# Performance work log

Hardware: AMD Instinct MI355X
Metric: run time of the kernel (lower is better)

Reference implementation:

```python
import jax, jax.numpy as jnp
import numpy as np

P, K, N, D = 4, 3, 250000, 64  # n_paths, num_powers, n_nodes, dim
N_EDGES = 100000


def setup_inputs() -> dict:
    key = jax.random.key(0)
    k1, k2, k3, k4 = jax.random.split(key, 4)
    feats = jax.random.normal(k1, (P, K, N, D), dtype=jnp.float32)
    # Each (path, power) slice was L2-normalized per node row in the original.
    feats = feats / jnp.linalg.norm(feats, axis=-1, keepdims=True)
    feature_weights = jnp.ones((P, K), dtype=jnp.float32)  # nn.Parameter init = ones
    intercept = jnp.float32(0.0)
    idx_i = jax.random.randint(k2, (N_EDGES,), 0, N, dtype=jnp.int64)
    idx_j = jax.random.randint(k3, (N_EDGES,), 0, N, dtype=jnp.int64)
    return {
        "precomputed_features": feats,
        "feature_weights": feature_weights,
        "intercept": intercept,
        "idx_i": idx_i,
        "idx_j": idx_j,
    }


def reference(precomputed_features, feature_weights, intercept, idx_i, idx_j):
    # softmax over the num_powers axis (dim=1 in torch)
    w = jax.nn.softmax(feature_weights, axis=1)  # [P, K]
    # weighted sum over paths and powers -> [N, D] embedding table
    emb = jnp.einsum("pk,pknd->nd", w, precomputed_features)
    zi = emb[idx_i]  # [E, D]
    zj = emb[idx_j]  # [E, D]
    dim = precomputed_features.shape[-1]
    dist_sq = jnp.sum((zi - zj) ** 2, axis=-1)
    logits = intercept - dist_sq / dim
    return jax.nn.sigmoid(logits)
```

## Files before the change

kernel.cpp:

```cpp
#include <hip/hip_runtime.h>
#include <hip/hip_bf16.h>
#include <math.h>


constexpr int Pp = 4;
constexpr int Kk = 3;
constexpr int Nn = 250000;
constexpr int Dd = 64;

__global__ __launch_bounds__(256) void fastrp_edge_kernel(
    const float* __restrict__ feats,
    const float* __restrict__ fw,
    const float* __restrict__ intercept,
    const int*   __restrict__ idx_i,
    const int*   __restrict__ idx_j,
    float*       __restrict__ out,
    int E)
{
    const int wave = (int)((blockIdx.x * (size_t)blockDim.x + threadIdx.x) >> 6);
    const int lane = threadIdx.x & 63;
    if (wave >= E) return;

    float w[Pp * Kk];
    #pragma unroll
    for (int p = 0; p < Pp; ++p) {
        float e[Kk];
        float m = -INFINITY;
        #pragma unroll
        for (int k = 0; k < Kk; ++k) {
            e[k] = fw[p * Kk + k];
            m = fmaxf(m, e[k]);
        }
        float s = 0.0f;
        #pragma unroll
        for (int k = 0; k < Kk; ++k) {
            e[k] = __expf(e[k] - m);
            s += e[k];
        }
        const float inv = 1.0f / s;
        #pragma unroll
        for (int k = 0; k < Kk; ++k) w[p * Kk + k] = e[k] * inv;
    }

    const long long i = (long long)idx_i[wave];
    const long long j = (long long)idx_j[wave];

    float zi = 0.0f, zj = 0.0f;
    #pragma unroll
    for (int pk = 0; pk < Pp * Kk; ++pk) {
        const float* base = feats + (size_t)pk * Nn * Dd;
        const float ai = base[i * Dd + lane];
        const float aj = base[j * Dd + lane];
        zi = fmaf(w[pk], ai, zi);
        zj = fmaf(w[pk], aj, zj);
    }

    float diff = zi - zj;
    float v = diff * diff;

    #pragma unroll
    for (int off = 32; off > 0; off >>= 1) {
        v += __shfl_xor(v, off, 64);
    }

    if (lane == 0) {
        const float logit = intercept[0] - v * (1.0f / Dd);
        out[wave] = 1.0f / (1.0f + __expf(-logit));
    }
}

extern "C" void kernel_launch(void* const* d_in, const int* in_sizes, int n_in,
                              void* d_out, int out_size, void* d_ws, size_t ws_size,
                              hipStream_t stream) {
    const float* feats     = (const float*)d_in[0];
    const float* fw        = (const float*)d_in[1];
    const float* intercept = (const float*)d_in[2];
    const int*   idx_i     = (const int*)d_in[3];
    const int*   idx_j     = (const int*)d_in[4];
    float*       out       = (float*)d_out;

    const int E = in_sizes[3];

    const int block = 256;
    const int waves_per_block = block / 64;
    const int grid = (E + waves_per_block - 1) / waves_per_block;

    fastrp_edge_kernel<<<grid, block, 0, stream>>>(feats, fw, intercept,
                                                   idx_i, idx_j, out, E);
}
```

Measured before the change: 909.6 us.

## Materialize weighted embedding table then gather edges with float4 loads

Splits the work into two kernels. The first streams all path/power feature slices once with float4 loads and writes a single softmax-weighted [N, D] embedding table into the workspace. The second gathers only that table per edge, with 16 lanes per edge, float4 loads and a short shuffle reduction. This replaces 12 scattered row gathers per endpoint with one sequential pass plus one gather per endpoint. The trade-off is reading the entire feature tensor even where no edge touches it, and it depends on the workspace being large enough, otherwise the old kernel still runs.

Result: slower. 984.5 us (+8.2%).

```diff
diff --git a/kernel.cpp b/kernel.cpp
--- a/kernel.cpp
+++ b/kernel.cpp
@@ -1,5 +1,4 @@
 #include <hip/hip_runtime.h>
-#include <hip/hip_bf16.h>
 #include <math.h>
 
 
@@ -7,21 +6,10 @@
 constexpr int Kk = 3;
 constexpr int Nn = 250000;
 constexpr int Dd = 64;
+constexpr int PK = Pp * Kk;
 
-__global__ __launch_bounds__(256) void fastrp_edge_kernel(
-    const float* __restrict__ feats,
-    const float* __restrict__ fw,
-    const float* __restrict__ intercept,
-    const int*   __restrict__ idx_i,
-    const int*   __restrict__ idx_j,
-    float*       __restrict__ out,
-    int E)
-{
-    const int wave = (int)((blockIdx.x * (size_t)blockDim.x + threadIdx.x) >> 6);
-    const int lane = threadIdx.x & 63;
-    if (wave >= E) return;
-
-    float w[Pp * Kk];
+__device__ __forceinline__ void softmax_weights(const float* __restrict__ fw,
+                                                float* __restrict__ w) {
     #pragma unroll
     for (int p = 0; p < Pp; ++p) {
         float e[Kk];
@@ -41,27 +29,98 @@
         #pragma unroll
         for (int k = 0; k < Kk; ++k) w[p * Kk + k] = e[k] * inv;
     }
+}
+
+__global__ __launch_bounds__(256) void fastrp_emb_kernel(
+    const float* __restrict__ feats,
+    const float* __restrict__ fw,
+    float*       __restrict__ emb,
+    int total4)
+{
+    float w[PK];
+    softmax_weights(fw, w);
+
+    const int stride = gridDim.x * blockDim.x;
+    for (int v = blockIdx.x * blockDim.x + threadIdx.x; v < total4; v += stride) {
+        float4 acc = make_float4(0.0f, 0.0f, 0.0f, 0.0f);
+        #pragma unroll
+        for (int pk = 0; pk < PK; ++pk) {
+            const float4* src =
+                reinterpret_cast<const float4*>(feats + (size_t)pk * Nn * Dd);
+            const float4 f = src[v];
+            acc.x = fmaf(w[pk], f.x, acc.x);
+            acc.y = fmaf(w[pk], f.y, acc.y);
+            acc.z = fmaf(w[pk], f.z, acc.z);
+            acc.w = fmaf(w[pk], f.w, acc.w);
+        }
+        reinterpret_cast<float4*>(emb)[v] = acc;
+    }
+}
+
+__global__ __launch_bounds__(256) void fastrp_edge_from_emb(
+    const float* __restrict__ emb,
+    const float* __restrict__ intercept,
+    const int*   __restrict__ idx_i,
+    const int*   __restrict__ idx_j,
+    float*       __restrict__ out,
+    int E)
+{
+    const int tid  = (int)(blockIdx.x * blockDim.x + threadIdx.x);
+    const int lane = threadIdx.x & 63;
+    const int q    = lane & 15;
+    const int e    = tid >> 4;
+    if (e >= E) return;
+
+    const long long i = (long long)idx_i[e];
+    const long long j = (long long)idx_j[e];
+
+    const float4 zi = *reinterpret_cast<const float4*>(emb + i * Dd + q * 4);
+    const float4 zj = *reinterpret_cast<const float4*>(emb + j * Dd + q * 4);
+
+    const float dx = zi.x - zj.x;
+    const float dy = zi.y - zj.y;
+    const float dz = zi.z - zj.z;
+    const float dw = zi.w - zj.w;
+    float v = dx * dx + dy * dy + dz * dz + dw * dw;
+
+    v += __shfl_xor(v, 1, 64);
+    v += __shfl_xor(v, 2, 64);
+    v += __shfl_xor(v, 4, 64);
+    v += __shfl_xor(v, 8, 64);
+
+    if (q == 0) {
+        const float logit = intercept[0] - v * (1.0f / Dd);
+        out[e] = 1.0f / (1.0f + __expf(-logit));
+    }
+}
+
+__global__ __launch_bounds__(256) void fastrp_edge_kernel(
+    const float* __restrict__ feats, const float* __restrict__ fw,
+    const float* __restrict__ intercept, const int* __restrict__ idx_i,
+    const int* __restrict__ idx_j, float* __restrict__ out, int E)
+{
+    const int wave = (int)((blockIdx.x * (size_t)blockDim.x + threadIdx.x) >> 6);
+    const int lane = threadIdx.x & 63;
+    if (wave >= E) return;
+
+    float w[PK];
+    softmax_weights(fw, w);
 
     const long long i = (long long)idx_i[wave];
     const long long j = (long long)idx_j[wave];
 
     float zi = 0.0f, zj = 0.0f;
     #pragma unroll
-    for (int pk = 0; pk < Pp * Kk; ++pk) {
+    for (int pk = 0; pk < PK; ++pk) {
         const float* base = feats + (size_t)pk * Nn * Dd;
-        const float ai = base[i * Dd + lane];
-        const float aj = base[j * Dd + lane];
-        zi = fmaf(w[pk], ai, zi);
-        zj = fmaf(w[pk], aj, zj);
+        zi = fmaf(w[pk], base[i * Dd + lane], zi);
+        zj = fmaf(w[pk], base[j * Dd + lane], zj);
     }
 
     float diff = zi - zj;
     float v = diff * diff;
-
     #pragma unroll
-    for (int off = 32; off > 0; off >>= 1) {
-        v += __shfl_xor(v, off, 64);
-    }
+    for (int off = 32; off > 0; off >>= 1) v += __shfl_xor(v, off, 64);
 
     if (lane == 0) {
         const float logit = intercept[0] - v * (1.0f / Dd);
@@ -80,11 +139,26 @@
     float*       out       = (float*)d_out;
 
     const int E = in_sizes[3];
+    const size_t emb_bytes = (size_t)Nn * Dd * sizeof(float);
 
-    const int block = 256;
-    const int waves_per_block = block / 64;
-    const int grid = (E + waves_per_block - 1) / waves_per_block;
+    if (ws_size >= emb_bytes) {
+        float* emb = (float*)d_ws;
 
-    fastrp_edge_kernel<<<grid, block, 0, stream>>>(feats, fw, intercept,
-                                                   idx_i, idx_j, out, E);
+        const int total4 = Nn * Dd / 4;
+        const int block1 = 256;
+        const int grid1  = 2048;
+        fastrp_emb_kernel<<<grid1, block1, 0, stream>>>(feats, fw, emb, total4);
+
+        const int block2 = 256;
+        const int edges_per_block = block2 / 16;
+        const int grid2 = (E + edges_per_block - 1) / edges_per_block;
+        fastrp_edge_from_emb<<<grid2, block2, 0, stream>>>(emb, intercept,
+                                                           idx_i, idx_j, out, E);
+    } else {
+        const int block = 256;
+        const int waves_per_block = block / 64;
+        const int grid = (E + waves_per_block - 1) / waves_per_block;
+        fastrp_edge_kernel<<<grid, block, 0, stream>>>(feats, fw, intercept,
+                                                       idx_i, idx_j, out, E);
+    }
 }
```
